# Kernel optimization log

Hardware: AMD Instinct MI355X
Metric: run time of the kernel (lower is better)

The kernel has to match this reference:

```python
import jax, jax.numpy as jnp
import numpy as np

N = 50000        # nodes
E = 1600000      # edges
NFEAT = 128      # node feature dim
NEDGE = 16       # raw edge feature dim
NHID = 128
NLAYER = 4
NGRAPH = 512
NOUT = 128
BN_EPS = 1e-5


def _bn(h, g, b):
    # eval-mode BatchNorm1d with running_mean=0, running_var=1
    return h * (g / jnp.sqrt(1.0 + BN_EPS)) + b


def setup_inputs() -> dict:
    key = jax.random.key(0)
    ks = jax.random.split(key, 24)
    s = 0.05
    inp = {
        "x": jax.random.normal(ks[0], (N, NFEAT), jnp.float32),
        "edge_index": jax.random.randint(ks[1], (2, E), 0, N, jnp.int64),
        "edge_attr": jax.random.normal(ks[2], (E, NEDGE), jnp.float32),
        "batch": jnp.sort(jax.random.randint(ks[3], (N,), 0, NGRAPH, jnp.int64)),
        # input encoder MLP (Linear + BN + ReLU)
        "in_W": jax.random.normal(ks[4], (NFEAT, NHID), jnp.float32) * s,
        "in_b": jnp.zeros((NHID,), jnp.float32),
        "in_g": jnp.ones((NHID,), jnp.float32),
        "in_beta": jnp.zeros((NHID,), jnp.float32),
        # per-layer edge encoder MLPs
        "edge_W": jax.random.normal(ks[5], (NLAYER, NEDGE, NHID), jnp.float32) * s,
        "edge_b": jnp.zeros((NLAYER, NHID), jnp.float32),
        "edge_g": jnp.ones((NLAYER, NHID), jnp.float32),
        "edge_beta": jnp.zeros((NLAYER, NHID), jnp.float32),
        # per-layer GINEConv linear (bias=False since bn=True) and eps
        "conv_W": jax.random.normal(ks[6], (NLAYER, NHID, NHID), jnp.float32) * s,
        "eps": jnp.zeros((NLAYER,), jnp.float32),
        # per-layer BatchNorm after conv
        "bn_g": jnp.ones((NLAYER, NHID), jnp.float32),
        "bn_b": jnp.zeros((NLAYER, NHID), jnp.float32),
        # output encoder: 2-layer MLP, norm after layer 1, no final activation
        "out_W1": jax.random.normal(ks[7], (NHID, NHID), jnp.float32) * s,
        "out_b1": jnp.zeros((NHID,), jnp.float32),
        "out_g1": jnp.ones((NHID,), jnp.float32),
        "out_beta1": jnp.zeros((NHID,), jnp.float32),
        "out_W2": jax.random.normal(ks[8], (NHID, NOUT), jnp.float32) * s,
        "out_b2": jnp.zeros((NOUT,), jnp.float32),
    }
    return inp


def reference(x, edge_index, edge_attr, batch,
              in_W, in_b, in_g, in_beta,
              edge_W, edge_b, edge_g, edge_beta,
              conv_W, eps, bn_g, bn_b,
              out_W1, out_b1, out_g1, out_beta1,
              out_W2, out_b2):
    # input encoder (MLP, 1 layer: Linear + BN + ReLU)
    h = jax.nn.relu(_bn(x @ in_W + in_b, in_g, in_beta))
    prev = h
    src, dst = edge_index[0], edge_index[1]
    for l in range(NLAYER):
        # edge encoder
        ea = jax.nn.relu(_bn(edge_attr @ edge_W[l] + edge_b[l], edge_g[l], edge_beta[l]))
        # GINEConv: messages relu(x_src + e), sum-aggregate to dst
        m = jax.nn.relu(h[src] + ea)                         # [E, NHID]
        agg = jax.ops.segment_sum(m, dst, num_segments=N)    # [N, NHID]
        h = ((1.0 + eps[l]) * h + agg) @ conv_W[l]
        h = jax.nn.relu(_bn(h, bn_g[l], bn_b[l]))            # dropout=0
        h = h + prev                                         # residual
        prev = h
    # add pooling over graphs
    pooled = jax.ops.segment_sum(h, batch, num_segments=NGRAPH)  # [NGRAPH, NHID]
    # output encoder: Linear+BN+ReLU, then Linear
    o = jax.nn.relu(_bn(pooled @ out_W1 + out_b1, out_g1, out_beta1))
    return o @ out_W2 + out_b2
```

## Files before the change

kernel.cpp:

```cpp
#include <hip/hip_runtime.h>
#include <stdint.h>

typedef uint32_t u32;
typedef _Float16 h2v __attribute__((ext_vector_type(2)));
typedef __attribute__((ext_vector_type(8))) short bf16x8;
typedef __attribute__((ext_vector_type(8))) _Float16 f16x8_t;
typedef __attribute__((ext_vector_type(4))) float f32x4;

#define NGRAPH 512

__device__ __forceinline__ float uif(u32 u) { return __builtin_bit_cast(float, u); }
__device__ __forceinline__ u32 fiu(float f) { return __builtin_bit_cast(u32, f); }
__device__ __forceinline__ unsigned short bf16r(float f) {
    return (unsigned short)((fiu(f) + 0x8000u) >> 16);
}
__device__ __forceinline__ u32 pack_bf16(float lo, float hi) {
    return ((fiu(lo) + 0x8000u) >> 16) | ((fiu(hi) + 0x8000u) & 0xFFFF0000u);
}
__device__ __forceinline__ u32 pkh(float a, float b) {
    unsigned short la = __builtin_bit_cast(unsigned short, (_Float16)a);
    unsigned short hb = __builtin_bit_cast(unsigned short, (_Float16)b);
    return (u32)la | ((u32)hb << 16);
}

__global__ __launch_bounds__(256) void prep_kernel(
    const float* __restrict__ in_b, const float* __restrict__ in_g, const float* __restrict__ in_beta,
    const float* __restrict__ edge_b, const float* __restrict__ edge_g, const float* __restrict__ edge_beta,
    const float* __restrict__ bn_g, const float* __restrict__ bn_b,
    const float* __restrict__ out_b1, const float* __restrict__ out_g1, const float* __restrict__ out_beta1,
    float* __restrict__ consts)
{
    int c = threadIdx.x;
    if (c >= 128) return;
    const float rs = rsqrtf(1.0f + 1e-5f);
    float es = in_g[c] * rs;
    consts[c]       = es;
    consts[128 + c] = in_b[c] * es + in_beta[c];
    for (int l = 0; l < 4; ++l) {
        float s = edge_g[l*128 + c] * rs;
        consts[256  + l*128 + c] = s;
        consts[768  + l*128 + c] = edge_b[l*128 + c] * s + edge_beta[l*128 + c];
        float bs = bn_g[l*128 + c] * rs;
        consts[1280 + l*128 + c] = bs;
        consts[1792 + l*128 + c] = bn_b[l*128 + c];
    }
    float s1 = out_g1[c] * rs;
    consts[2304 + c] = s1;
    consts[2432 + c] = out_b1[c] * s1 + out_beta1[c];
}

__global__ __launch_bounds__(256) void wfrag_kernel(
    const float* __restrict__ edge_W, const float* __restrict__ edge_g,
    _Float16* __restrict__ wfrag)
{
    int idx = blockIdx.x*blockDim.x + threadIdx.x;
    if (idx >= 4*8*64*8) return;
    int j = idx & 7, lane = (idx >> 3) & 63, t = (idx >> 9) & 7, l = idx >> 12;
    int k = (lane >> 4)*8 + j;
    int n = t*16 + (lane & 15);
    const float rs = rsqrtf(1.0f + 1e-5f);
    wfrag[idx] = (k < 16)
        ? (_Float16)(edge_W[(l*16 + k)*128 + n] * (edge_g[l*128 + n] * rs))
        : (_Float16)0.f;
}

__global__ __launch_bounds__(256) void prepw_kernel(
    const float* __restrict__ in_W, const float* __restrict__ conv_W,
    unsigned short* __restrict__ WtAll)
{
    for (int idx = blockIdx.x*blockDim.x + threadIdx.x; idx < 5*128*128;
         idx += gridDim.x*blockDim.x) {
        int w = idx >> 14, rem = idx & 16383;
        int nn = rem >> 7, kk = rem & 127;
        const float* S = (w == 0) ? in_W : conv_W + (size_t)(w-1)*16384;
        WtAll[idx] = bf16r(S[kk*128 + nn]);
    }
}

__global__ __launch_bounds__(256) void xconv_kernel(
    const float* __restrict__ x, u32* __restrict__ x16, int n4)
{
    for (int i = blockIdx.x*blockDim.x + threadIdx.x; i < n4;
         i += gridDim.x*blockDim.x) {
        float4 v = *(const float4*)(x + (size_t)i*4);
        uint2 o; o.x = pack_bf16(v.x, v.y); o.y = pack_bf16(v.z, v.w);
        *(uint2*)(x16 + (size_t)i*2) = o;
    }
}

__global__ __launch_bounds__(256) void count_kernel(
    const int* __restrict__ dst, int E, int* __restrict__ cnt)
{
    for (int e = blockIdx.x*blockDim.x + threadIdx.x; e < E; e += gridDim.x*blockDim.x)
        atomicAdd(&cnt[dst[e]], 1);
}

__global__ __launch_bounds__(1024) void scan_kernel(
    const int* __restrict__ cnt, int n, int E,
    int* __restrict__ offs, int* __restrict__ cursor)
{
    __shared__ int sh[1024];
    const int t = threadIdx.x;
    const int chunk = (n + 1023) >> 10;
    const int lo = t * chunk;
    const int hi = min(n, lo + chunk);
    int s = 0;
    for (int i = lo; i < hi; ++i) s += cnt[i];
    sh[t] = s;
    __syncthreads();
    for (int d = 1; d < 1024; d <<= 1) {
        int v = (t >= d) ? sh[t - d] : 0;
        __syncthreads();
        sh[t] += v;
        __syncthreads();
    }
    int base = sh[t] - s;
    for (int i = lo; i < hi; ++i) { int c = cnt[i]; offs[i] = base; cursor[i] = base; base += c; }
    if (t == 1023) offs[n] = E;
}

__global__ __launch_bounds__(256) void scatter_perm_kernel(
    const int* __restrict__ dst, int E,
    int* __restrict__ cursor, int* __restrict__ perm)
{
    for (int e = blockIdx.x*blockDim.x + threadIdx.x; e < E; e += gridDim.x*blockDim.x) {
        int p = atomicAdd(&cursor[dst[e]], 1);
        perm[p] = e;
    }
}

__global__ __launch_bounds__(256) void apply_perm_kernel(
    const int* __restrict__ perm, const int* __restrict__ src,
    const float* __restrict__ attr, int E,
    int* __restrict__ srcoff, uint4* __restrict__ attrp)
{
    for (int p = blockIdx.x*blockDim.x + threadIdx.x; p < E; p += gridDim.x*blockDim.x) {
        const int e = perm[p];
        srcoff[p] = src[e] * 256;
        const float4* ar = (const float4*)(attr + (size_t)e*16);
        float4 v0 = ar[0], v1 = ar[1], v2 = ar[2], v3 = ar[3];
        uint4 o0, o1;
        o0.x = pkh(v0.x, v0.y); o0.y = pkh(v0.z, v0.w);
        o0.z = pkh(v1.x, v1.y); o0.w = pkh(v1.z, v1.w);
        o1.x = pkh(v2.x, v2.y); o1.y = pkh(v2.z, v2.w);
        o1.z = pkh(v3.x, v3.y); o1.w = pkh(v3.z, v3.w);
        attrp[2*(size_t)p] = o0; attrp[2*(size_t)p + 1] = o1;
    }
}

__global__ __launch_bounds__(256) void goff_kernel(
    const int* __restrict__ batch, int n, int* __restrict__ goff)
{
    int g = blockIdx.x*blockDim.x + threadIdx.x;
    if (g > NGRAPH) return;
    if (g == NGRAPH) { goff[NGRAPH] = n; return; }
    int lo = 0, hi = n;
    while (lo < hi) { int m = (lo + hi) >> 1; if (batch[m] < g) lo = m + 1; else hi = m; }
    goff[g] = lo;
}

__global__ __launch_bounds__(256) void eagg2_kernel(
    const uint4* __restrict__ attrp, const int* __restrict__ offs,
    const _Float16* __restrict__ wfrag, const float* __restrict__ consts,
    int lbase, u32* __restrict__ eagg, int n)
{
    __shared__ float eabuf[4][128];
    const int wave = threadIdx.x >> 6, lane = threadIdx.x & 63;
    const int c0 = lane * 2;
    const int l15 = lane & 15, l4 = lane >> 4;

    f16x8_t bw[16];
    #pragma unroll
    for (int lt = 0; lt < 16; ++lt)
        bw[lt] = *(const f16x8_t*)(wfrag + ((size_t)(lbase*8 + lt)*64 + lane)*8);
    float of[16];
    #pragma unroll
    for (int ll = 0; ll < 2; ++ll)
        #pragma unroll
        for (int t = 0; t < 8; ++t)
            of[ll*8 + t] = consts[768 + (lbase + ll)*128 + t*16 + l15];
    const f16x8_t az = (f16x8_t)(_Float16)0.f;

    for (int node = blockIdx.x*4 + wave; node < n; node += gridDim.x*4) {
        const int beg = offs[node], end = offs[node+1];
        float easum[16];
        #pragma unroll
        for (int lt = 0; lt < 16; ++lt) easum[lt] = 0.f;

        for (int g = beg; g < end; g += 16) {
            const int rem = end - g;
            f16x8_t a = az;
            if (l4 < 2) {
                int e = g + l15; if (e > end - 1) e = end - 1;
                a = *(const f16x8_t*)((const char*)attrp + (size_t)e*32 + l4*16);
            }
            if (rem >= 16) {
                #pragma unroll
                for (int lt = 0; lt < 16; ++lt) {
                    f32x4 d = __builtin_amdgcn_mfma_f32_16x16x32_f16(
                        a, bw[lt], f32x4{0.f,0.f,0.f,0.f}, 0, 0, 0);
                    #pragma unroll
                    for (int r = 0; r < 4; ++r)
                        easum[lt] += fmaxf(d[r] + of[lt], 0.f);
                }
            } else {
                #pragma unroll
                for (int lt = 0; lt < 16; ++lt) {
                    f32x4 d = __builtin_amdgcn_mfma_f32_16x16x32_f16(
                        a, bw[lt], f32x4{0.f,0.f,0.f,0.f}, 0, 0, 0);
                    #pragma unroll
                    for (int r = 0; r < 4; ++r) {
                        float y = fmaxf(d[r] + of[lt], 0.f);
                        easum[lt] += ((l4*4 + r) < rem) ? y : 0.f;
                    }
                }
            }
        }
        #pragma unroll
        for (int ll = 0; ll < 2; ++ll) {
            #pragma unroll
            for (int t = 0; t < 8; ++t) {
                float v = easum[ll*8 + t];
                v += __shfl_xor(v, 16);
                v += __shfl_xor(v, 32);
                if (l4 == 0) eabuf[wave][t*16 + l15] = v;
            }
            float2 ea2 = *(float2*)&eabuf[wave][c0];
            eagg[(size_t)(lbase + ll)*n*64 + (size_t)node*64 + lane] =
                pack_bf16(ea2.x, ea2.y);
        }
    }
}

__global__ __launch_bounds__(256) void hagg_kernel(
    const char* __restrict__ hb, const int* __restrict__ srcoff,
    const int* __restrict__ offs, const u32* __restrict__ eagg_l,
    const float* __restrict__ epsp, int layer,
    u32* __restrict__ C16, int n)
{
    const int wave = threadIdx.x >> 6, lane = threadIdx.x & 63;
    const int lane4 = lane * 4;
    const float epsv = 1.0f + epsp[layer];
    for (int node = blockIdx.x*4 + wave; node < n; node += gridDim.x*4) {
        const int beg = offs[node], end = offs[node+1];
        float acc0 = 0.f, acc1 = 0.f;
        int i = beg;
        for (; i + 7 < end; i += 8) {
            const int iu = __builtin_amdgcn_readfirstlane(i);
            const int4 sa = *(const int4*)(srcoff + iu);
            const int4 sb = *(const int4*)(srcoff + iu + 4);
            const u32 h0 = *(const u32*)(hb + sa.x + lane4);
            const u32 h1 = *(const u32*)(hb + sa.y + lane4);
            const u32 h2 = *(const u32*)(hb + sa.z + lane4);
            const u32 h3 = *(const u32*)(hb + sa.w + lane4);
            const u32 h4 = *(const u32*)(hb + sb.x + lane4);
            const u32 h5 = *(const u32*)(hb + sb.y + lane4);
            const u32 h6 = *(const u32*)(hb + sb.z + lane4);
            const u32 h7 = *(const u32*)(hb + sb.w + lane4);
            acc0 += uif(h0 << 16); acc1 += uif(h0 & 0xFFFF0000u);
            acc0 += uif(h1 << 16); acc1 += uif(h1 & 0xFFFF0000u);
            acc0 += uif(h2 << 16); acc1 += uif(h2 & 0xFFFF0000u);
            acc0 += uif(h3 << 16); acc1 += uif(h3 & 0xFFFF0000u);
            acc0 += uif(h4 << 16); acc1 += uif(h4 & 0xFFFF0000u);
            acc0 += uif(h5 << 16); acc1 += uif(h5 & 0xFFFF0000u);
            acc0 += uif(h6 << 16); acc1 += uif(h6 & 0xFFFF0000u);
            acc0 += uif(h7 << 16); acc1 += uif(h7 & 0xFFFF0000u);
        }
        for (; i + 3 < end; i += 4) {
            const int iu = __builtin_amdgcn_readfirstlane(i);
            const int4 sa = *(const int4*)(srcoff + iu);
            const u32 h0 = *(const u32*)(hb + sa.x + lane4);
            const u32 h1 = *(const u32*)(hb + sa.y + lane4);
            const u32 h2 = *(const u32*)(hb + sa.z + lane4);
            const u32 h3 = *(const u32*)(hb + sa.w + lane4);
            acc0 += uif(h0 << 16); acc1 += uif(h0 & 0xFFFF0000u);
            acc0 += uif(h1 << 16); acc1 += uif(h1 & 0xFFFF0000u);
            acc0 += uif(h2 << 16); acc1 += uif(h2 & 0xFFFF0000u);
            acc0 += uif(h3 << 16); acc1 += uif(h3 & 0xFFFF0000u);
        }
        for (; i < end; ++i) {
            const int iu = __builtin_amdgcn_readfirstlane(i);
            const u32 h0 = *(const u32*)(hb + srcoff[iu] + lane4);
            acc0 += uif(h0 << 16); acc1 += uif(h0 & 0xFFFF0000u);
        }
        const u32 eg = eagg_l[(size_t)node*64 + lane];
        const u32 hn = *(const u32*)(hb + (size_t)node*256 + lane4);
        float t0 = fmaf(epsv, uif(hn << 16),          acc0 + uif(eg << 16));
        float t1 = fmaf(epsv, uif(hn & 0xFFFF0000u),  acc1 + uif(eg & 0xFFFF0000u));
        C16[(size_t)node*64 + lane] = pack_bf16(t0, t1);
    }
}

__global__ __launch_bounds__(256) void conv_mfma_kernel(
    const unsigned short* X16, int M,
    const unsigned short* __restrict__ Wt,
    const float* __restrict__ scale, const float* __restrict__ off,
    const unsigned short* __restrict__ resid16,
    unsigned short* out16, int do_relu)
{
    __shared__ unsigned short Ws[128*128];
    for (int i = threadIdx.x*8; i < 128*128; i += 256*8) {
        int row = i >> 7;
        int bo = (i & 127) * 2;
        int4 v = *(const int4*)(Wt + i);
        *(int4*)((char*)Ws + row*256 + (bo ^ ((row & 7) << 4))) = v;
    }
    __syncthreads();
    const int wave = threadIdx.x >> 6, lane = threadIdx.x & 63;
    const int row0 = blockIdx.x*64 + wave*16;
    const int l15 = lane & 15, l4 = lane >> 4;
    int arow = row0 + l15; if (arow > M-1) arow = M-1;
    const unsigned short* ap = X16 + (size_t)arow*128 + l4*8;
    f32x4 acc[8];
    #pragma unroll
    for (int t = 0; t < 8; ++t) acc[t] = f32x4{0.f, 0.f, 0.f, 0.f};
    #pragma unroll
    for (int ks = 0; ks < 4; ++ks) {
        bf16x8 a = *(const bf16x8*)(ap + ks*32);
        #pragma unroll
        for (int t = 0; t < 8; ++t) {
            int brow = t*16 + l15;
            int bo = ks*64 + l4*16;
            bf16x8 b = *(const bf16x8*)((const char*)Ws + brow*256 + (bo ^ ((brow & 7) << 4)));
            acc[t] = __builtin_amdgcn_mfma_f32_16x16x32_bf16(a, b, acc[t], 0, 0, 0);
        }
    }
    #pragma unroll
    for (int t = 0; t < 8; ++t) {
        int col = t*16 + l15;
        float sc = scale[col], of = off[col];
        #pragma unroll
        for (int r = 0; r < 4; ++r) {
            int row = row0 + l4*4 + r;
            if (row < M) {
                float y = fmaf(acc[t][r], sc, of);
                if (do_relu) y = fmaxf(y, 0.f);
                if (resid16) y += uif((u32)resid16[(size_t)row*128 + col] << 16);
                out16[(size_t)row*128 + col] = bf16r(y);
            }
        }
    }
}

__global__ __launch_bounds__(256) void pool_kernel(
    const u32* __restrict__ h16, const int* __restrict__ goff,
    float* __restrict__ pooled)
{
    const int wave = threadIdx.x >> 6, lane = threadIdx.x & 63;
    const int g = blockIdx.x*4 + wave;
    if (g >= NGRAPH) return;
    float ax = 0.f, ay = 0.f;
    const int beg = goff[g], end = goff[g+1];
    for (int node = beg; node < end; ++node) {
        u32 v = h16[(size_t)node*64 + lane];
        ax += uif(v << 16); ay += uif(v & 0xFFFF0000u);
    }
    *(float2*)&pooled[g*128 + lane*2] = make_float2(ax, ay);
}

__global__ __launch_bounds__(256) void gemm128_kernel(
    const float* __restrict__ in, int rows,
    const float* __restrict__ W,
    const float* __restrict__ scale, const float* __restrict__ off,
    float* out, int do_relu)
{
    __shared__ float Wsh[128*128];
    for (int i = threadIdx.x*4; i < 128*128; i += 256*4)
        *(float4*)&Wsh[i] = *(const float4*)&W[i];
    __syncthreads();
    const int wave = threadIdx.x >> 6, lane = threadIdx.x & 63;
    const int c0 = lane * 2;
    const float sc0 = scale ? scale[c0]   : 1.0f;
    const float sc1 = scale ? scale[c0+1] : 1.0f;
    const float of0 = off ? off[c0]   : 0.0f;
    const float of1 = off ? off[c0+1] : 0.0f;
    for (int rp = blockIdx.x*4 + wave; rp*2 < rows; rp += gridDim.x*4) {
        const int row0 = __builtin_amdgcn_readfirstlane(rp * 2);
        const float* xr = in + (size_t)row0 * 128;
        float a00 = 0.f, a01 = 0.f, a10 = 0.f, a11 = 0.f;
        #pragma unroll 8
        for (int k = 0; k < 128; ++k) {
            float x0 = xr[k];
            float x1 = xr[128 + k];
            float2 w = *(const float2*)&Wsh[k*128 + c0];
            a00 = fmaf(x0, w.x, a00); a01 = fmaf(x0, w.y, a01);
            a10 = fmaf(x1, w.x, a10); a11 = fmaf(x1, w.y, a11);
        }
        float y00 = fmaf(a00, sc0, of0), y01 = fmaf(a01, sc1, of1);
        float y10 = fmaf(a10, sc0, of0), y11 = fmaf(a11, sc1, of1);
        if (do_relu) {
            y00 = fmaxf(y00, 0.f); y01 = fmaxf(y01, 0.f);
            y10 = fmaxf(y10, 0.f); y11 = fmaxf(y11, 0.f);
        }
        *(float2*)&out[(size_t)row0*128 + c0]     = make_float2(y00, y01);
        *(float2*)&out[(size_t)(row0+1)*128 + c0] = make_float2(y10, y11);
    }
}

extern "C" void kernel_launch(void* const* d_in, const int* in_sizes, int n_in,
                              void* d_out, int out_size, void* d_ws, size_t ws_size,
                              hipStream_t stream)
{
    const float* x         = (const float*)d_in[0];
    const int*   eidx      = (const int*)d_in[1];
    const float* eattr     = (const float*)d_in[2];
    const int*   batch     = (const int*)d_in[3];
    const float* in_W      = (const float*)d_in[4];
    const float* in_b      = (const float*)d_in[5];
    const float* in_g      = (const float*)d_in[6];
    const float* in_beta   = (const float*)d_in[7];
    const float* edge_W    = (const float*)d_in[8];
    const float* edge_b    = (const float*)d_in[9];
    const float* edge_g    = (const float*)d_in[10];
    const float* edge_beta = (const float*)d_in[11];
    const float* conv_W    = (const float*)d_in[12];
    const float* epsp      = (const float*)d_in[13];
    const float* bn_g      = (const float*)d_in[14];
    const float* bn_b      = (const float*)d_in[15];
    const float* out_W1    = (const float*)d_in[16];
    const float* out_b1    = (const float*)d_in[17];
    const float* out_g1    = (const float*)d_in[18];
    const float* out_beta1 = (const float*)d_in[19];
    const float* out_W2    = (const float*)d_in[20];
    const float* out_b2    = (const float*)d_in[21];

    const int N = in_sizes[0] / 128;
    const int E = in_sizes[1] / 2;
    const int* src = eidx;
    const int* dst = eidx + E;

    char* ws = (char*)d_ws;
    size_t o = 0;
    auto alloc = [&](size_t bytes) { void* p = ws + o; o = (o + bytes + 255) & ~(size_t)255; return p; };
    unsigned short* P    = (unsigned short*)alloc((size_t)N * 128 * 2);
    unsigned short* Q    = (unsigned short*)alloc((size_t)N * 128 * 2);
    uint4* attrp         = (uint4*)alloc((size_t)E * 32);
    int*   srcoff        = (int*)alloc((size_t)E * 4);
    int*   perm          = (int*)alloc((size_t)E * 4);
    u32*   eagg          = (u32*)alloc((size_t)N * 64 * 4 * 4);
    int*   offs          = (int*)alloc((size_t)(N + 1) * 4);
    int*   cursor        = (int*)alloc((size_t)N * 4);
    int*   cnt           = (int*)alloc((size_t)N * 4);
    int*   goff          = (int*)alloc((NGRAPH + 1) * 4);
    float* pooled        = (float*)alloc(NGRAPH * 128 * 4);
    float* o1            = (float*)alloc(NGRAPH * 128 * 4);
    float* consts        = (float*)alloc(2560 * 4);
    _Float16* wfrag      = (_Float16*)alloc(4 * 8 * 64 * 8 * 2);
    unsigned short* WtAll = (unsigned short*)alloc(5 * 128 * 128 * 2);

    prep_kernel<<<1, 256, 0, stream>>>(in_b, in_g, in_beta,
                                       edge_b, edge_g, edge_beta,
                                       bn_g, bn_b, out_b1, out_g1, out_beta1,
                                       consts);
    wfrag_kernel<<<64, 256, 0, stream>>>(edge_W, edge_g, wfrag);
    prepw_kernel<<<80, 256, 0, stream>>>(in_W, conv_W, WtAll);
    xconv_kernel<<<2048, 256, 0, stream>>>(x, (u32*)Q, N * 32);

    (void)hipMemsetAsync(cnt, 0, (size_t)N * 4, stream);
    count_kernel<<<2048, 256, 0, stream>>>(dst, E, cnt);
    scan_kernel<<<1, 1024, 0, stream>>>(cnt, N, E, offs, cursor);
    scatter_perm_kernel<<<2048, 256, 0, stream>>>(dst, E, cursor, perm);
    apply_perm_kernel<<<2048, 256, 0, stream>>>(perm, src, eattr, E, srcoff, attrp);
    goff_kernel<<<3, 256, 0, stream>>>(batch, N, goff);

    const int gblocks = (N + 63) / 64;
    conv_mfma_kernel<<<gblocks, 256, 0, stream>>>(Q, N, WtAll,
                                                  consts, consts + 128,
                                                  nullptr, Q, 1);
    eagg2_kernel<<<2048, 256, 0, stream>>>(attrp, offs, wfrag, consts, 0, eagg, N);
    eagg2_kernel<<<2048, 256, 0, stream>>>(attrp, offs, wfrag, consts, 2, eagg, N);

    unsigned short* cur = Q;
    unsigned short* oth = P;
    for (int l = 0; l < 4; ++l) {
        hagg_kernel<<<2048, 256, 0, stream>>>((const char*)cur, srcoff, offs,
                                              eagg + (size_t)l * N * 64,
                                              epsp, l, (u32*)oth, N);
        conv_mfma_kernel<<<gblocks, 256, 0, stream>>>(oth, N,
                                                      WtAll + (size_t)(1 + l)*16384,
                                                      consts + 1280 + l*128,
                                                      consts + 1792 + l*128,
                                                      cur, oth, 1);
        unsigned short* t = cur; cur = oth; oth = t;
    }

    pool_kernel<<<128, 256, 0, stream>>>((const u32*)cur, goff, pooled);

    gemm128_kernel<<<64, 256, 0, stream>>>(pooled, NGRAPH, out_W1,
                                           consts + 2304, consts + 2432, o1, 1);
    gemm128_kernel<<<64, 256, 0, stream>>>(o1, NGRAPH, out_W2,
                                           nullptr, out_b2, (float*)d_out, 0);
}
```

Before: 971.1 us.

## Fuse edge permutation into single scatter writing interleaved edge records

Measured after the change: 939.5 us. 3.3% less time.

```diff
diff --git a/kernel.cpp b/kernel.cpp
--- a/kernel.cpp
+++ b/kernel.cpp
@@ -8,6 +8,7 @@
 typedef __attribute__((ext_vector_type(4))) float f32x4;
 
 #define NGRAPH 512
+#define RSTRIDE 48
 
 __device__ __forceinline__ float uif(u32 u) { return __builtin_bit_cast(float, u); }
 __device__ __forceinline__ u32 fiu(float f) { return __builtin_bit_cast(u32, f); }
@@ -119,24 +120,13 @@
     if (t == 1023) offs[n] = E;
 }
 
-__global__ __launch_bounds__(256) void scatter_perm_kernel(
-    const int* __restrict__ dst, int E,
-    int* __restrict__ cursor, int* __restrict__ perm)
+__global__ __launch_bounds__(256) void scatter_kernel(
+    const int* __restrict__ src, const int* __restrict__ dst,
+    const float* __restrict__ attr, int E,
+    int* __restrict__ cursor, char* __restrict__ rec)
 {
     for (int e = blockIdx.x*blockDim.x + threadIdx.x; e < E; e += gridDim.x*blockDim.x) {
         int p = atomicAdd(&cursor[dst[e]], 1);
-        perm[p] = e;
-    }
-}
-
-__global__ __launch_bounds__(256) void apply_perm_kernel(
-    const int* __restrict__ perm, const int* __restrict__ src,
-    const float* __restrict__ attr, int E,
-    int* __restrict__ srcoff, uint4* __restrict__ attrp)
-{
-    for (int p = blockIdx.x*blockDim.x + threadIdx.x; p < E; p += gridDim.x*blockDim.x) {
-        const int e = perm[p];
-        srcoff[p] = src[e] * 256;
         const float4* ar = (const float4*)(attr + (size_t)e*16);
         float4 v0 = ar[0], v1 = ar[1], v2 = ar[2], v3 = ar[3];
         uint4 o0, o1;
@@ -144,7 +134,10 @@
         o0.z = pkh(v1.x, v1.y); o0.w = pkh(v1.z, v1.w);
         o1.x = pkh(v2.x, v2.y); o1.y = pkh(v2.z, v2.w);
         o1.z = pkh(v3.x, v3.y); o1.w = pkh(v3.z, v3.w);
-        attrp[2*(size_t)p] = o0; attrp[2*(size_t)p + 1] = o1;
+        char* r = rec + (size_t)p * RSTRIDE;
+        *(uint4*)(r)      = o0;
+        *(uint4*)(r + 16) = o1;
+        *(uint4*)(r + 32) = make_uint4((u32)(src[e] * 256), 0u, 0u, 0u);
     }
 }
 
@@ -160,7 +153,7 @@
 }
 
 __global__ __launch_bounds__(256) void eagg2_kernel(
-    const uint4* __restrict__ attrp, const int* __restrict__ offs,
+    const char* __restrict__ rec, const int* __restrict__ offs,
     const _Float16* __restrict__ wfrag, const float* __restrict__ consts,
     int lbase, u32* __restrict__ eagg, int n)
 {
@@ -192,7 +185,7 @@
             f16x8_t a = az;
             if (l4 < 2) {
                 int e = g + l15; if (e > end - 1) e = end - 1;
-                a = *(const f16x8_t*)((const char*)attrp + (size_t)e*32 + l4*16);
+                a = *(const f16x8_t*)(rec + (size_t)e*RSTRIDE + l4*16);
             }
             if (rem >= 16) {
                 #pragma unroll
@@ -226,14 +219,14 @@
                 if (l4 == 0) eabuf[wave][t*16 + l15] = v;
             }
             float2 ea2 = *(float2*)&eabuf[wave][c0];
-            eagg[(size_t)(lbase + ll)*n*64 + (size_t)node*64 + lane] =
+            eagg[(size_t)ll*n*64 + (size_t)node*64 + lane] =
                 pack_bf16(ea2.x, ea2.y);
         }
     }
 }
 
 __global__ __launch_bounds__(256) void hagg_kernel(
-    const char* __restrict__ hb, const int* __restrict__ srcoff,
+    const char* __restrict__ hb, const char* __restrict__ rec,
     const int* __restrict__ offs, const u32* __restrict__ eagg_l,
     const float* __restrict__ epsp, int layer,
     u32* __restrict__ C16, int n)
@@ -247,16 +240,23 @@
         int i = beg;
         for (; i + 7 < end; i += 8) {
             const int iu = __builtin_amdgcn_readfirstlane(i);
-            const int4 sa = *(const int4*)(srcoff + iu);
-            const int4 sb = *(const int4*)(srcoff + iu + 4);
-            const u32 h0 = *(const u32*)(hb + sa.x + lane4);
-            const u32 h1 = *(const u32*)(hb + sa.y + lane4);
-            const u32 h2 = *(const u32*)(hb + sa.z + lane4);
-            const u32 h3 = *(const u32*)(hb + sa.w + lane4);
-            const u32 h4 = *(const u32*)(hb + sb.x + lane4);
-            const u32 h5 = *(const u32*)(hb + sb.y + lane4);
-            const u32 h6 = *(const u32*)(hb + sb.z + lane4);
-            const u32 h7 = *(const u32*)(hb + sb.w + lane4);
+            const char* rb = rec + (size_t)iu*RSTRIDE + 32;
+            const int so0 = *(const int*)(rb);
+            const int so1 = *(const int*)(rb + RSTRIDE);
+            const int so2 = *(const int*)(rb + 2*RSTRIDE);
+            const int so3 = *(const int*)(rb + 3*RSTRIDE);
+            const int so4 = *(const int*)(rb + 4*RSTRIDE);
+            const int so5 = *(const int*)(rb + 5*RSTRIDE);
+            const int so6 = *(const int*)(rb + 6*RSTRIDE);
+            const int so7 = *(const int*)(rb + 7*RSTRIDE);
+            const u32 h0 = *(const u32*)(hb + so0 + lane4);
+            const u32 h1 = *(const u32*)(hb + so1 + lane4);
+            const u32 h2 = *(const u32*)(hb + so2 + lane4);
+            const u32 h3 = *(const u32*)(hb + so3 + lane4);
+            const u32 h4 = *(const u32*)(hb + so4 + lane4);
+            const u32 h5 = *(const u32*)(hb + so5 + lane4);
+            const u32 h6 = *(const u32*)(hb + so6 + lane4);
+            const u32 h7 = *(const u32*)(hb + so7 + lane4);
             acc0 += uif(h0 << 16); acc1 += uif(h0 & 0xFFFF0000u);
             acc0 += uif(h1 << 16); acc1 += uif(h1 & 0xFFFF0000u);
             acc0 += uif(h2 << 16); acc1 += uif(h2 & 0xFFFF0000u);
@@ -268,11 +268,15 @@
         }
         for (; i + 3 < end; i += 4) {
             const int iu = __builtin_amdgcn_readfirstlane(i);
-            const int4 sa = *(const int4*)(srcoff + iu);
-            const u32 h0 = *(const u32*)(hb + sa.x + lane4);
-            const u32 h1 = *(const u32*)(hb + sa.y + lane4);
-            const u32 h2 = *(const u32*)(hb + sa.z + lane4);
-            const u32 h3 = *(const u32*)(hb + sa.w + lane4);
+            const char* rb = rec + (size_t)iu*RSTRIDE + 32;
+            const int so0 = *(const int*)(rb);
+            const int so1 = *(const int*)(rb + RSTRIDE);
+            const int so2 = *(const int*)(rb + 2*RSTRIDE);
+            const int so3 = *(const int*)(rb + 3*RSTRIDE);
+            const u32 h0 = *(const u32*)(hb + so0 + lane4);
+            const u32 h1 = *(const u32*)(hb + so1 + lane4);
+            const u32 h2 = *(const u32*)(hb + so2 + lane4);
+            const u32 h3 = *(const u32*)(hb + so3 + lane4);
             acc0 += uif(h0 << 16); acc1 += uif(h0 & 0xFFFF0000u);
             acc0 += uif(h1 << 16); acc1 += uif(h1 & 0xFFFF0000u);
             acc0 += uif(h2 << 16); acc1 += uif(h2 & 0xFFFF0000u);
@@ -280,7 +284,8 @@
         }
         for (; i < end; ++i) {
             const int iu = __builtin_amdgcn_readfirstlane(i);
-            const u32 h0 = *(const u32*)(hb + srcoff[iu] + lane4);
+            const int so0 = *(const int*)(rec + (size_t)iu*RSTRIDE + 32);
+            const u32 h0 = *(const u32*)(hb + so0 + lane4);
             acc0 += uif(h0 << 16); acc1 += uif(h0 & 0xFFFF0000u);
         }
         const u32 eg = eagg_l[(size_t)node*64 + lane];
@@ -434,10 +439,8 @@
     auto alloc = [&](size_t bytes) { void* p = ws + o; o = (o + bytes + 255) & ~(size_t)255; return p; };
     unsigned short* P    = (unsigned short*)alloc((size_t)N * 128 * 2);
     unsigned short* Q    = (unsigned short*)alloc((size_t)N * 128 * 2);
-    uint4* attrp         = (uint4*)alloc((size_t)E * 32);
-    int*   srcoff        = (int*)alloc((size_t)E * 4);
-    int*   perm          = (int*)alloc((size_t)E * 4);
-    u32*   eagg          = (u32*)alloc((size_t)N * 64 * 4 * 4);
+    char*  rec           = (char*)alloc((size_t)E * RSTRIDE);
+    u32*   eagg          = (u32*)alloc((size_t)N * 64 * 2 * 4);
     int*   offs          = (int*)alloc((size_t)(N + 1) * 4);
     int*   cursor        = (int*)alloc((size_t)N * 4);
     int*   cnt           = (int*)alloc((size_t)N * 4);
@@ -459,22 +462,22 @@
     (void)hipMemsetAsync(cnt, 0, (size_t)N * 4, stream);
     count_kernel<<<2048, 256, 0, stream>>>(dst, E, cnt);
     scan_kernel<<<1, 1024, 0, stream>>>(cnt, N, E, offs, cursor);
-    scatter_perm_kernel<<<2048, 256, 0, stream>>>(dst, E, cursor, perm);
-    apply_perm_kernel<<<2048, 256, 0, stream>>>(perm, src, eattr, E, srcoff, attrp);
+    scatter_kernel<<<2048, 256, 0, stream>>>(src, dst, eattr, E, cursor, rec);
     goff_kernel<<<3, 256, 0, stream>>>(batch, N, goff);
 
     const int gblocks = (N + 63) / 64;
     conv_mfma_kernel<<<gblocks, 256, 0, stream>>>(Q, N, WtAll,
                                                   consts, consts + 128,
                                                   nullptr, Q, 1);
-    eagg2_kernel<<<2048, 256, 0, stream>>>(attrp, offs, wfrag, consts, 0, eagg, N);
-    eagg2_kernel<<<2048, 256, 0, stream>>>(attrp, offs, wfrag, consts, 2, eagg, N);
 
     unsigned short* cur = Q;
     unsigned short* oth = P;
     for (int l = 0; l < 4; ++l) {
-        hagg_kernel<<<2048, 256, 0, stream>>>((const char*)cur, srcoff, offs,
-                                              eagg + (size_t)l * N * 64,
+        if ((l & 1) == 0)
+            eagg2_kernel<<<2048, 256, 0, stream>>>(rec, offs, wfrag, consts,
+                                                   l, eagg, N);
+        hagg_kernel<<<2048, 256, 0, stream>>>((const char*)cur, rec, offs,
+                                              eagg + (size_t)(l & 1) * N * 64,
                                               epsp, l, (u32*)oth, N);
         conv_mfma_kernel<<<gblocks, 256, 0, stream>>>(oth, N,
                                                       WtAll + (size_t)(1 + l)*16384,
```

## Fuse edge permutation into scatter with packed records and interleave edge aggregation

Applied to the files above, without the earlier changes.

Result: faster. 900.0 us (-7.3%).

```diff
diff --git a/kernel.cpp b/kernel.cpp
--- a/kernel.cpp
+++ b/kernel.cpp
@@ -8,6 +8,7 @@
 typedef __attribute__((ext_vector_type(4))) float f32x4;
 
 #define NGRAPH 512
+#define RSTRIDE 48
 
 __device__ __forceinline__ float uif(u32 u) { return __builtin_bit_cast(float, u); }
 __device__ __forceinline__ u32 fiu(float f) { return __builtin_bit_cast(u32, f); }
@@ -119,24 +120,13 @@
     if (t == 1023) offs[n] = E;
 }
 
-__global__ __launch_bounds__(256) void scatter_perm_kernel(
-    const int* __restrict__ dst, int E,
-    int* __restrict__ cursor, int* __restrict__ perm)
+__global__ __launch_bounds__(256) void scatter_kernel(
+    const int* __restrict__ src, const int* __restrict__ dst,
+    const float* __restrict__ attr, int E,
+    int* __restrict__ cursor, char* __restrict__ rec)
 {
     for (int e = blockIdx.x*blockDim.x + threadIdx.x; e < E; e += gridDim.x*blockDim.x) {
         int p = atomicAdd(&cursor[dst[e]], 1);
-        perm[p] = e;
-    }
-}
-
-__global__ __launch_bounds__(256) void apply_perm_kernel(
-    const int* __restrict__ perm, const int* __restrict__ src,
-    const float* __restrict__ attr, int E,
-    int* __restrict__ srcoff, uint4* __restrict__ attrp)
-{
-    for (int p = blockIdx.x*blockDim.x + threadIdx.x; p < E; p += gridDim.x*blockDim.x) {
-        const int e = perm[p];
-        srcoff[p] = src[e] * 256;
         const float4* ar = (const float4*)(attr + (size_t)e*16);
         float4 v0 = ar[0], v1 = ar[1], v2 = ar[2], v3 = ar[3];
         uint4 o0, o1;
@@ -144,8 +134,18 @@
         o0.z = pkh(v1.x, v1.y); o0.w = pkh(v1.z, v1.w);
         o1.x = pkh(v2.x, v2.y); o1.y = pkh(v2.z, v2.w);
         o1.z = pkh(v3.x, v3.y); o1.w = pkh(v3.z, v3.w);
-        attrp[2*(size_t)p] = o0; attrp[2*(size_t)p + 1] = o1;
-    }
+        char* r = rec + (size_t)p * RSTRIDE;
+        *(uint4*)(r)      = o0;
+        *(uint4*)(r + 16) = o1;
+        *(uint4*)(r + 32) = make_uint4((u32)(src[e] * 256), 0u, 0u, 0u);
+    }
+}
+
+__global__ __launch_bounds__(256) void extract_srcoff_kernel(
+    const char* __restrict__ rec, int E, int* __restrict__ srcoff)
+{
+    for (int p = blockIdx.x*blockDim.x + threadIdx.x; p < E; p += gridDim.x*blockDim.x)
+        srcoff[p] = *(const int*)(rec + (size_t)p*RSTRIDE + 32);
 }
 
 __global__ __launch_bounds__(256) void goff_kernel(
@@ -160,7 +160,7 @@
 }
 
 __global__ __launch_bounds__(256) void eagg2_kernel(
-    const uint4* __restrict__ attrp, const int* __restrict__ offs,
+    const char* __restrict__ rec, const int* __restrict__ offs,
     const _Float16* __restrict__ wfrag, const float* __restrict__ consts,
     int lbase, u32* __restrict__ eagg, int n)
 {
@@ -192,7 +192,7 @@
             f16x8_t a = az;
             if (l4 < 2) {
                 int e = g + l15; if (e > end - 1) e = end - 1;
-                a = *(const f16x8_t*)((const char*)attrp + (size_t)e*32 + l4*16);
+                a = *(const f16x8_t*)(rec + (size_t)e*RSTRIDE + l4*16);
             }
             if (rem >= 16) {
                 #pragma unroll
@@ -226,7 +226,7 @@
                 if (l4 == 0) eabuf[wave][t*16 + l15] = v;
             }
             float2 ea2 = *(float2*)&eabuf[wave][c0];
-            eagg[(size_t)(lbase + ll)*n*64 + (size_t)node*64 + lane] =
+            eagg[(size_t)ll*n*64 + (size_t)node*64 + lane] =
                 pack_bf16(ea2.x, ea2.y);
         }
     }
@@ -434,10 +434,9 @@
     auto alloc = [&](size_t bytes) { void* p = ws + o; o = (o + bytes + 255) & ~(size_t)255; return p; };
     unsigned short* P    = (unsigned short*)alloc((size_t)N * 128 * 2);
     unsigned short* Q    = (unsigned short*)alloc((size_t)N * 128 * 2);
-    uint4* attrp         = (uint4*)alloc((size_t)E * 32);
+    char*  rec           = (char*)alloc((size_t)E * RSTRIDE);
     int*   srcoff        = (int*)alloc((size_t)E * 4);
-    int*   perm          = (int*)alloc((size_t)E * 4);
-    u32*   eagg          = (u32*)alloc((size_t)N * 64 * 4 * 4);
+    u32*   eagg          = (u32*)alloc((size_t)N * 64 * 2 * 4);
     int*   offs          = (int*)alloc((size_t)(N + 1) * 4);
     int*   cursor        = (int*)alloc((size_t)N * 4);
     int*   cnt           = (int*)alloc((size_t)N * 4);
@@ -459,22 +458,23 @@
     (void)hipMemsetAsync(cnt, 0, (size_t)N * 4, stream);
     count_kernel<<<2048, 256, 0, stream>>>(dst, E, cnt);
     scan_kernel<<<1, 1024, 0, stream>>>(cnt, N, E, offs, cursor);
-    scatter_perm_kernel<<<2048, 256, 0, stream>>>(dst, E, cursor, perm);
-    apply_perm_kernel<<<2048, 256, 0, stream>>>(perm, src, eattr, E, srcoff, attrp);
+    scatter_kernel<<<2048, 256, 0, stream>>>(src, dst, eattr, E, cursor, rec);
+    extract_srcoff_kernel<<<2048, 256, 0, stream>>>(rec, E, srcoff);
     goff_kernel<<<3, 256, 0, stream>>>(batch, N, goff);
 
     const int gblocks = (N + 63) / 64;
     conv_mfma_kernel<<<gblocks, 256, 0, stream>>>(Q, N, WtAll,
                                                   consts, consts + 128,
                                                   nullptr, Q, 1);
-    eagg2_kernel<<<2048, 256, 0, stream>>>(attrp, offs, wfrag, consts, 0, eagg, N);
-    eagg2_kernel<<<2048, 256, 0, stream>>>(attrp, offs, wfrag, consts, 2, eagg, N);
 
     unsigned short* cur = Q;
     unsigned short* oth = P;
     for (int l = 0; l < 4; ++l) {
+        if ((l & 1) == 0)
+            eagg2_kernel<<<2048, 256, 0, stream>>>(rec, offs, wfrag, consts,
+                                                   l, eagg, N);
         hagg_kernel<<<2048, 256, 0, stream>>>((const char*)cur, srcoff, offs,
-                                              eagg + (size_t)l * N * 64,
+                                              eagg + (size_t)(l & 1) * N * 64,
                                               epsp, l, (u32*)oth, N);
         conv_mfma_kernel<<<gblocks, 256, 0, stream>>>(oth, N,
                                                       WtAll + (size_t)(1 + l)*16384,
```
